# Kernel tuning notes

Hardware: AMD Instinct MI355X
Metric: run time of the kernel (lower is better)

## Reference

```python
import jax, jax.numpy as jnp
import numpy as np
import math

IN_C = 768
CA = 384
K1 = (3, 1, 1)
K2 = (1, 3, 3)
K3 = (3, 3, 3)


def _dwconv3d(x, w, b):
    # x: [B, Ca, T, H, W]; w: [Ca, 1, kt, kh, kw]; depthwise (groups = Ca)
    pads = [(k // 2, k // 2) for k in w.shape[2:]]
    y = jax.lax.conv_general_dilated(
        x, w, window_strides=(1, 1, 1), padding=pads,
        feature_group_count=x.shape[1],
        dimension_numbers=("NCDHW", "OIDHW", "NCDHW"))
    return y + b[None, :, None, None, None]


def setup_inputs() -> dict:
    key = jax.random.key(0)
    ks = jax.random.split(key, 12)
    s = 0.02
    x = jax.random.normal(ks[0], (128, 197, IN_C), dtype=jnp.float32)
    fc1_w = jax.random.normal(ks[1], (CA, IN_C), dtype=jnp.float32) * s
    fc1_b = jnp.zeros((CA,), dtype=jnp.float32)
    conv1_w = jax.random.normal(ks[2], (CA, 1) + K1, dtype=jnp.float32) * s
    conv1_b = jax.random.normal(ks[3], (CA,), dtype=jnp.float32) * s
    conv2_w = jax.random.normal(ks[4], (CA, 1) + K2, dtype=jnp.float32) * s
    conv2_b = jax.random.normal(ks[5], (CA,), dtype=jnp.float32) * s
    conv3_w = jax.random.normal(ks[6], (CA, 1) + K3, dtype=jnp.float32) * s
    conv3_b = jax.random.normal(ks[7], (CA,), dtype=jnp.float32) * s
    proj_w = jax.random.normal(ks[8], (CA, 1) + K1, dtype=jnp.float32) * s
    proj_b = jax.random.normal(ks[9], (CA,), dtype=jnp.float32) * s
    fc2_w = jax.random.normal(ks[10], (IN_C, CA), dtype=jnp.float32) * s
    fc2_b = jnp.zeros((IN_C,), dtype=jnp.float32)
    return {
        "x": x, "fc1_w": fc1_w, "fc1_b": fc1_b,
        "conv1_w": conv1_w, "conv1_b": conv1_b,
        "conv2_w": conv2_w, "conv2_b": conv2_b,
        "conv3_w": conv3_w, "conv3_b": conv3_b,
        "proj_w": proj_w, "proj_b": proj_b,
        "fc2_w": fc2_w, "fc2_b": fc2_b,
        "T": 16,
    }


def reference(x, fc1_w, fc1_b, conv1_w, conv1_b, conv2_w, conv2_b,
              conv3_w, conv3_b, proj_w, proj_b, fc2_w, fc2_b, T):
    BT, L, C = x.shape
    B = BT // T
    H = W = round(math.sqrt(L - 1))
    Ca = fc1_w.shape[0]
    x_id = x
    # drop CLS token, project down: [BT, L-1, Ca]
    h = jnp.einsum("blc,ac->bla", x[:, 1:, :], fc1_w) + fc1_b
    # [B, Ca, T, H, W]
    h = h.reshape(B, T, H, W, Ca).transpose(0, 4, 1, 2, 3)
    identity = h
    h = (_dwconv3d(h, conv1_w, conv1_b)
         + _dwconv3d(h, conv2_w, conv2_b)
         + _dwconv3d(h, conv3_w, conv3_b)) / 3.0
    h = h + identity
    h = h + _dwconv3d(h, proj_w, proj_b)
    # back to tokens: [BT, L-1, Ca]
    h = h.transpose(0, 2, 3, 4, 1).reshape(BT, L - 1, Ca)
    h = jnp.einsum("bla,ca->blc", h, fc2_w) + fc2_b
    return x_id.at[:, 1:, :].add(h)
```

## Files before the change

kernel.cpp:

```cpp
#include <hip/hip_runtime.h>
#include <cstdint>

typedef __bf16 bf16_t;
typedef __bf16 bf16x4 __attribute__((ext_vector_type(4)));
typedef __bf16 bf16x8 __attribute__((ext_vector_type(8)));
typedef float f32x4 __attribute__((ext_vector_type(4)));

#define BT_   128
#define LTOK  197
#define CIN   768
#define CA_   384
#define TT    16
#define HH    14
#define NTOK  25088

__device__ __forceinline__ void gl_lds16(const void* g, void* l) {
  __builtin_amdgcn_global_load_lds(
      (const __attribute__((address_space(1))) unsigned int*)g,
      (__attribute__((address_space(3))) unsigned int*)l,
      16, 0, 0);
}

#define SBAR() do { __builtin_amdgcn_sched_barrier(0); \
                    __builtin_amdgcn_s_barrier(); \
                    __builtin_amdgcn_sched_barrier(0); } while (0)

__global__ void prep_weights_kernel(
    const float* __restrict__ c1w, const float* __restrict__ c1b,
    const float* __restrict__ c2w, const float* __restrict__ c2b,
    const float* __restrict__ c3w, const float* __restrict__ c3b,
    const float* __restrict__ projw,
    bf16_t* __restrict__ Wtb,
    float* __restrict__ beff,
    float* __restrict__ pwt) {
  int a = blockIdx.x * blockDim.x + threadIdx.x;
  if (a >= CA_) return;
  for (int dt = 0; dt < 3; dt++)
    for (int dh = 0; dh < 3; dh++)
      for (int dw = 0; dw < 3; dw++) {
        float v = c3w[a*27 + dt*9 + dh*3 + dw];
        if (dh == 1 && dw == 1) v += c1w[a*3 + dt];
        if (dt == 1)            v += c2w[a*9 + dh*3 + dw];
        v *= (1.0f/3.0f);
        if (dt == 1 && dh == 1 && dw == 1) v += 1.0f;
        Wtb[((dt*3+dh)*3+dw)*CA_ + a] = (bf16_t)v;
      }
  beff[a] = (c1b[a] + c2b[a] + c3b[a]) * (1.0f/3.0f);
  pwt[0*CA_ + a] = projw[a*3 + 0];
  pwt[1*CA_ + a] = projw[a*3 + 1];
  pwt[2*CA_ + a] = projw[a*3 + 2];
}

__global__ __launch_bounds__(256) void convert_w_kernel(
    const float* __restrict__ fc1w, const float* __restrict__ fc2w,
    const float* __restrict__ x, float* __restrict__ out,
    bf16_t* __restrict__ W1, bf16_t* __restrict__ W2,
    bf16_t* __restrict__ xb) {
  const int NW1 = CA_*CIN/4;
  const int NW2 = CIN*CA_/4;
  const int NX  = BT_*LTOK*CIN/4;
  const int total = NW1 + NW2 + NX;
  for (int i = blockIdx.x*256 + threadIdx.x; i < total; i += gridDim.x*256) {
    if (i < NW1) {
      float4 v = ((const float4*)fc1w)[i];
      bf16x4 b; b[0]=(bf16_t)v.x; b[1]=(bf16_t)v.y; b[2]=(bf16_t)v.z; b[3]=(bf16_t)v.w;
      *(bf16x4*)(W1 + (size_t)i*4) = b;
    } else if (i < NW1 + NW2) {
      int j = i - NW1;
      float4 v = ((const float4*)fc2w)[j];
      bf16x4 b; b[0]=(bf16_t)v.x; b[1]=(bf16_t)v.y; b[2]=(bf16_t)v.z; b[3]=(bf16_t)v.w;
      *(bf16x4*)(W2 + (size_t)j*4) = b;
    } else {
      int j = i - NW1 - NW2;
      int row = j / 192;
      int c4  = j - row*192;
      int l   = row % 197;
      float4 v = ((const float4*)x)[(size_t)j];
      if (l == 0) {
        ((float4*)out)[(size_t)j] = v;
      } else {
        int tok = (row/197)*196 + (l - 1);
        bf16x4 b; b[0]=(bf16_t)v.x; b[1]=(bf16_t)v.y; b[2]=(bf16_t)v.z; b[3]=(bf16_t)v.w;
        *(bf16x4*)(xb + (size_t)tok*CIN + c4*4) = b;
      }
    }
  }
}

__global__ __launch_bounds__(256) void gemm1_kernel(
    const bf16_t* __restrict__ xb, const bf16_t* __restrict__ W1,
    const float* __restrict__ fc1b, bf16_t* __restrict__ H0) {
  __shared__ bf16_t Alds[3][128*32];
  __shared__ bf16_t Blds[3][128*32];
  const int tid  = threadIdx.x;
  const int lane = tid & 63;
  const int wave = tid >> 6;
  const int bm = blockIdx.x, bn = blockIdx.y;

  const bf16_t* asrc0 = xb + (size_t)(bm*128 + (tid>>2))*CIN + (tid&3)*8;
  const bf16_t* asrc1 = asrc0 + (size_t)64*CIN;
  const bf16_t* bsrc0 = W1 + (size_t)(bn*128 + (tid>>2))*CIN + (tid&3)*8;
  const bf16_t* bsrc1 = bsrc0 + (size_t)64*CIN;
  const int off0 = tid*8;
  const int off1 = (tid+256)*8;

  const int quad = lane >> 4;
  const int r16  = lane & 15;
  const int wm = (wave >> 1) * 64;
  const int wn = (wave & 1) * 64;

  f32x4 acc[4][4] = {};

#define G1_G(S, K) do { \
    gl_lds16(asrc0 + (K), &Alds[S][off0]); \
    gl_lds16(asrc1 + (K), &Alds[S][off1]); \
    gl_lds16(bsrc0 + (K), &Blds[S][off0]); \
    gl_lds16(bsrc1 + (K), &Blds[S][off1]); } while (0)
#define G1_M(S) do { bf16x8 af_[4], bf_[4]; \
    _Pragma("unroll") \
    for (int mt = 0; mt < 4; mt++) \
      af_[mt] = *(const bf16x8*)&Alds[S][(wm + mt*16 + r16)*32 + quad*8]; \
    _Pragma("unroll") \
    for (int nt = 0; nt < 4; nt++) \
      bf_[nt] = *(const bf16x8*)&Blds[S][(wn + nt*16 + r16)*32 + quad*8]; \
    _Pragma("unroll") \
    for (int mt = 0; mt < 4; mt++) \
      _Pragma("unroll") \
      for (int nt = 0; nt < 4; nt++) \
        acc[mt][nt] = __builtin_amdgcn_mfma_f32_16x16x32_bf16(af_[mt], bf_[nt], acc[mt][nt], 0, 0, 0); \
  } while (0)

  G1_G(0, 0);
  G1_G(1, 32);
  asm volatile("s_waitcnt vmcnt(4)" ::: "memory");
  SBAR();

  #pragma unroll 1
  for (int ii = 0; ii < 7; ii++) {
    #pragma unroll
    for (int j = 0; j < 3; j++) {
      const int i = ii*3 + j;
      G1_G((j + 2) % 3, (i + 2)*32);
      G1_M(j);
      asm volatile("s_waitcnt vmcnt(4)" ::: "memory");
      SBAR();
    }
  }
  G1_G(2, 23*32);
  G1_M(0);
  asm volatile("s_waitcnt vmcnt(4)" ::: "memory");
  SBAR();
  G1_M(1);
  asm volatile("s_waitcnt vmcnt(0)" ::: "memory");
  SBAR();
  G1_M(2);

  #pragma unroll
  for (int nt = 0; nt < 4; nt++) {
    const int col = bn*128 + wn + nt*16 + r16;
    const float bias = fc1b[col];
    #pragma unroll
    for (int mt = 0; mt < 4; mt++) {
      const int row0 = bm*128 + wm + mt*16 + quad*4;
      #pragma unroll
      for (int rg = 0; rg < 4; rg++)
        H0[(size_t)(row0 + rg)*CA_ + col] = (bf16_t)(acc[mt][nt][rg] + bias);
    }
  }
#undef G1_G
#undef G1_M
}

__global__ __launch_bounds__(192) void conv_kernel(
    const bf16_t* __restrict__ H0,
    const bf16_t* __restrict__ Wtb,
    const float* __restrict__ beff,
    const float* __restrict__ pwt,
    const float* __restrict__ pb,
    bf16_t* __restrict__ Z) {
  __shared__ bf16_t Wlds[27*CA_];
  __shared__ float  ybuf[2][2][CA_];

  const int tid = threadIdx.x;
  {
    const uint4* src = (const uint4*)Wtb;
    uint4* dst = (uint4*)Wlds;
    #pragma unroll
    for (int i = 0; i < 7; i++) {
      int idx = tid + i*192;
      if (idx < 27*CA_/8) dst[idx] = src[idx];
    }
  }

  const int blk  = blockIdx.x;
  const int b    = blk & 7;
  const int pair = blk >> 3;
  const int cg   = tid % 48;
  const int ct   = tid / 48;
  const int col  = ct >> 1;
  const int th   = ct & 1;
  const int hw   = pair*2 + col;
  const int h    = hw / HH, w = hw % HH;
  const int c0   = cg * 8;
  const int t0   = th * 8;

  float y[8][8];
  {
    f32x4 bv0 = *(const f32x4*)(beff + c0);
    f32x4 bv1 = *(const f32x4*)(beff + c0 + 4);
    #pragma unroll
    for (int i = 0; i < 8; i++) {
      #pragma unroll
      for (int c = 0; c < 4; c++) { y[i][c] = bv0[c]; y[i][c+4] = bv1[c]; }
    }
  }

  __syncthreads();

  const size_t rowstride = (size_t)196*CA_;
  const bf16_t* base_t0 = H0 + ((size_t)(b*TT + t0)*196)*CA_ + c0;
  const int tau_e_off = th ? -1 : 8;

  for (int j = 0; j < 9; j++) {
    const int dh = j / 3, dw = j - dh*3;
    const int h2 = h + dh - 1, w2 = w + dw - 1;
    const bool ok = ((unsigned)h2 < HH) && ((unsigned)w2 < HH);
    const int sp = ok ? (h2*HH + w2) : hw;
    const float m = ok ? 1.0f : 0.0f;

    const bf16x8 wv0 = *(const bf16x8*)&Wlds[(0*9+j)*CA_ + c0];
    const bf16x8 wv1 = *(const bf16x8*)&Wlds[(1*9+j)*CA_ + c0];
    const bf16x8 wv2 = *(const bf16x8*)&Wlds[(2*9+j)*CA_ + c0];
    float mw0[8], mw1[8], mw2[8];
    #pragma unroll
    for (int c = 0; c < 8; c++) {
      mw0[c] = m * (float)wv0[c];
      mw1[c] = m * (float)wv1[c];
      mw2[c] = m * (float)wv2[c];
    }

    const bf16_t* tp = base_t0 + (size_t)sp*CA_;
    bf16x8 gv[8];
    #pragma unroll
    for (int i = 0; i < 8; i++)
      gv[i] = *(const bf16x8*)(tp + (ptrdiff_t)i*(ptrdiff_t)rowstride);
    const bf16x8 ge = *(const bf16x8*)(tp + (ptrdiff_t)tau_e_off*(ptrdiff_t)rowstride);

    #pragma unroll
    for (int i = 0; i < 8; i++) {
      float gf[8];
      #pragma unroll
      for (int c = 0; c < 8; c++) gf[c] = (float)gv[i][c];
      #pragma unroll
      for (int c = 0; c < 8; c++) y[i][c] += gf[c]*mw1[c];
      if (i > 0) {
        #pragma unroll
        for (int c = 0; c < 8; c++) y[i-1][c] += gf[c]*mw2[c];
      }
      if (i < 7) {
        #pragma unroll
        for (int c = 0; c < 8; c++) y[i+1][c] += gf[c]*mw0[c];
      }
    }
    {
      float gf[8];
      #pragma unroll
      for (int c = 0; c < 8; c++) gf[c] = (float)ge[c];
      if (th) {
        #pragma unroll
        for (int c = 0; c < 8; c++) y[0][c] += gf[c]*mw0[c];
      } else {
        #pragma unroll
        for (int c = 0; c < 8; c++) y[7][c] += gf[c]*mw2[c];
      }
    }
  }

  #pragma unroll
  for (int c = 0; c < 8; c++) ybuf[col][th][c0+c] = th ? y[0][c] : y[7][c];
  __syncthreads();
  float yedge[8];
  #pragma unroll
  for (int c = 0; c < 8; c++) yedge[c] = ybuf[col][1-th][c0+c];

  float p0[8], p1[8], p2[8], pbv[8];
  {
    f32x4 a0 = *(const f32x4*)(pwt + 0*CA_ + c0), a1 = *(const f32x4*)(pwt + 0*CA_ + c0 + 4);
    f32x4 b0 = *(const f32x4*)(pwt + 1*CA_ + c0), b1 = *(const f32x4*)(pwt + 1*CA_ + c0 + 4);
    f32x4 d0 = *(const f32x4*)(pwt + 2*CA_ + c0), d1 = *(const f32x4*)(pwt + 2*CA_ + c0 + 4);
    f32x4 e0 = *(const f32x4*)(pb + c0),          e1 = *(const f32x4*)(pb + c0 + 4);
    #pragma unroll
    for (int c = 0; c < 4; c++) {
      p0[c]=a0[c]; p0[c+4]=a1[c];
      p1[c]=b0[c]; p1[c+4]=b1[c];
      p2[c]=d0[c]; p2[c+4]=d1[c];
      pbv[c]=e0[c]; pbv[c+4]=e1[c];
    }
  }

  bf16_t* zbase = Z + ((size_t)(b*TT + t0)*196 + hw)*CA_ + c0;
  #pragma unroll
  for (int i = 0; i < 8; i++) {
    bf16x8 zo;
    #pragma unroll
    for (int c = 0; c < 8; c++) {
      const float ym = (i > 0) ? y[i-1][c] : (th ? yedge[c] : 0.f);
      const float yp = (i < 7) ? y[i+1][c] : (th ? 0.f : yedge[c]);
      const float z  = y[i][c] + pbv[c] + p0[c]*ym + p1[c]*y[i][c] + p2[c]*yp;
      zo[c] = (bf16_t)z;
    }
    *(bf16x8*)(zbase + (size_t)i*rowstride) = zo;
  }
}

__global__ __launch_bounds__(256) void gemm2_kernel(
    const bf16_t* __restrict__ Z, const bf16_t* __restrict__ W2,
    const float* __restrict__ fc2b, const float* __restrict__ x,
    float* __restrict__ out) {
  __shared__ bf16_t Alds[3][128*32];
  __shared__ bf16_t Blds[3][128*32];
  const int tid  = threadIdx.x;
  const int lane = tid & 63;
  const int wave = tid >> 6;
  const int bm = blockIdx.x, bn = blockIdx.y;

  const bf16_t* asrc0 = Z  + (size_t)(bm*128 + (tid>>2))*CA_ + (tid&3)*8;
  const bf16_t* asrc1 = asrc0 + (size_t)64*CA_;
  const bf16_t* bsrc0 = W2 + (size_t)(bn*128 + (tid>>2))*CA_ + (tid&3)*8;
  const bf16_t* bsrc1 = bsrc0 + (size_t)64*CA_;
  const int off0 = tid*8;
  const int off1 = (tid+256)*8;

  const int quad = lane >> 4;
  const int r16  = lane & 15;
  const int wm = (wave >> 1) * 64;
  const int wn = (wave & 1) * 64;

  f32x4 acc[4][4] = {};

#define G2_G(S, K) do { \
    gl_lds16(asrc0 + (K), &Alds[S][off0]); \
    gl_lds16(asrc1 + (K), &Alds[S][off1]); \
    gl_lds16(bsrc0 + (K), &Blds[S][off0]); \
    gl_lds16(bsrc1 + (K), &Blds[S][off1]); } while (0)
#define G2_M(S) do { bf16x8 af_[4], bf_[4]; \
    _Pragma("unroll") \
    for (int mt = 0; mt < 4; mt++) \
      af_[mt] = *(const bf16x8*)&Alds[S][(wm + mt*16 + r16)*32 + quad*8]; \
    _Pragma("unroll") \
    for (int nt = 0; nt < 4; nt++) \
      bf_[nt] = *(const bf16x8*)&Blds[S][(wn + nt*16 + r16)*32 + quad*8]; \
    _Pragma("unroll") \
    for (int mt = 0; mt < 4; mt++) \
      _Pragma("unroll") \
      for (int nt = 0; nt < 4; nt++) \
        acc[mt][nt] = __builtin_amdgcn_mfma_f32_16x16x32_bf16(af_[mt], bf_[nt], acc[mt][nt], 0, 0, 0); \
  } while (0)

  G2_G(0, 0);
  G2_G(1, 32);
  asm volatile("s_waitcnt vmcnt(4)" ::: "memory");
  SBAR();

  #pragma unroll 1
  for (int ii = 0; ii < 3; ii++) {
    #pragma unroll
    for (int j = 0; j < 3; j++) {
      const int i = ii*3 + j;
      G2_G((j + 2) % 3, (i + 2)*32);
      G2_M(j);
      asm volatile("s_waitcnt vmcnt(4)" ::: "memory");
      SBAR();
    }
  }
  G2_G(2, 11*32);
  G2_M(0);
  asm volatile("s_waitcnt vmcnt(4)" ::: "memory");
  SBAR();
  G2_M(1);
  asm volatile("s_waitcnt vmcnt(0)" ::: "memory");
  SBAR();
  G2_M(2);

  #pragma unroll
  for (int nt = 0; nt < 4; nt++) {
    const int col = bn*128 + wn + nt*16 + r16;
    const float bias = fc2b[col];
    #pragma unroll
    for (int mt = 0; mt < 4; mt++) {
      #pragma unroll
      for (int rg = 0; rg < 4; rg++) {
        const int tok = bm*128 + wm + mt*16 + quad*4 + rg;
        const int bt  = tok / 196;
        const size_t o = (size_t)(tok + bt + 1)*CIN + col;
        out[o] = x[o] + acc[mt][nt][rg] + bias;
      }
    }
  }
#undef G2_G
#undef G2_M
}

extern "C" void kernel_launch(void* const* d_in, const int* in_sizes, int n_in,
                              void* d_out, int out_size, void* d_ws, size_t ws_size,
                              hipStream_t stream) {
  (void)in_sizes; (void)n_in; (void)out_size; (void)ws_size;
  const float* x    = (const float*)d_in[0];
  const float* fc1w = (const float*)d_in[1];
  const float* fc1b = (const float*)d_in[2];
  const float* c1w  = (const float*)d_in[3];
  const float* c1b  = (const float*)d_in[4];
  const float* c2w  = (const float*)d_in[5];
  const float* c2b  = (const float*)d_in[6];
  const float* c3w  = (const float*)d_in[7];
  const float* c3b  = (const float*)d_in[8];
  const float* pw   = (const float*)d_in[9];
  const float* pb   = (const float*)d_in[10];
  const float* fc2w = (const float*)d_in[11];
  const float* fc2b = (const float*)d_in[12];
  float* out = (float*)d_out;

  char* ws = (char*)d_ws;
  bf16_t* W1   = (bf16_t*)(ws);
  bf16_t* W2   = (bf16_t*)(ws + 589824);
  bf16_t* Wtb  = (bf16_t*)(ws + 1179648);
  float*  beff = (float*) (ws + 1200384);
  float*  pwt  = (float*) (ws + 1201920);
  bf16_t* xb   = (bf16_t*)(ws + 1206528);
  bf16_t* Z    = (bf16_t*)(ws + 1206528);
  bf16_t* H0   = (bf16_t*)(ws + 39741696);

  prep_weights_kernel<<<dim3(2), dim3(192), 0, stream>>>(
      c1w, c1b, c2w, c2b, c3w, c3b, pw, Wtb, beff, pwt);
  convert_w_kernel<<<dim3(4096), dim3(256), 0, stream>>>(fc1w, fc2w, x, out, W1, W2, xb);
  gemm1_kernel<<<dim3(196, 3), dim3(256), 0, stream>>>(xb, W1, fc1b, H0);
  conv_kernel<<<dim3(784), dim3(192), 0, stream>>>(H0, Wtb, beff, pwt, pb, Z);
  gemm2_kernel<<<dim3(196, 6), dim3(256), 0, stream>>>(Z, W2, fc2b, x, out);
}
```

Baseline: 279.5 us.

## Pre-swizzle GEMM weights into MFMA fragment layout and load B directly to registers

The weight conversion now writes fc1/fc2 into a fragment-ordered layout, so each lane can fetch its MFMA B operand with one contiguous 16-byte global load. Both GEMMs drop the B tile from LDS and load B fragments straight into registers each k-step. This halves LDS traffic and the global-to-LDS copies per stage and frees LDS for occupancy. In exchange, B loads now come from global or L2 memory with less time to hide their latency, and each of the two waves in a column pair fetches the same weights.

```diff
diff --git a/kernel.cpp b/kernel.cpp
--- a/kernel.cpp
+++ b/kernel.cpp
@@ -54,7 +54,7 @@
 __global__ __launch_bounds__(256) void convert_w_kernel(
     const float* __restrict__ fc1w, const float* __restrict__ fc2w,
     const float* __restrict__ x, float* __restrict__ out,
-    bf16_t* __restrict__ W1, bf16_t* __restrict__ W2,
+    bf16_t* __restrict__ W1f, bf16_t* __restrict__ W2f,
     bf16_t* __restrict__ xb) {
   const int NW1 = CA_*CIN/4;
   const int NW2 = CIN*CA_/4;
@@ -62,14 +62,21 @@
   const int total = NW1 + NW2 + NX;
   for (int i = blockIdx.x*256 + threadIdx.x; i < total; i += gridDim.x*256) {
     if (i < NW1) {
-      float4 v = ((const float4*)fc1w)[i];
+      int e = i*4, f = e >> 9, t = e & 511, l = t >> 3, jb = t & 7;
+      int ch = f / 24, cb = f - ch*24;
+      int col = cb*16 + (l & 15);
+      int k   = ch*32 + ((l >> 4) << 3) + jb;
+      float4 v = *(const float4*)(fc1w + (size_t)col*CIN + k);
       bf16x4 b; b[0]=(bf16_t)v.x; b[1]=(bf16_t)v.y; b[2]=(bf16_t)v.z; b[3]=(bf16_t)v.w;
-      *(bf16x4*)(W1 + (size_t)i*4) = b;
+      *(bf16x4*)(W1f + e) = b;
     } else if (i < NW1 + NW2) {
-      int j = i - NW1;
-      float4 v = ((const float4*)fc2w)[j];
+      int e = (i - NW1)*4, f = e >> 9, t = e & 511, l = t >> 3, jb = t & 7;
+      int ch = f / 48, cb = f - ch*48;
+      int col = cb*16 + (l & 15);
+      int k   = ch*32 + ((l >> 4) << 3) + jb;
+      float4 v = *(const float4*)(fc2w + (size_t)col*CA_ + k);
       bf16x4 b; b[0]=(bf16_t)v.x; b[1]=(bf16_t)v.y; b[2]=(bf16_t)v.z; b[3]=(bf16_t)v.w;
-      *(bf16x4*)(W2 + (size_t)j*4) = b;
+      *(bf16x4*)(W2f + e) = b;
     } else {
       int j = i - NW1 - NW2;
       int row = j / 192;
@@ -88,10 +95,9 @@
 }
 
 __global__ __launch_bounds__(256) void gemm1_kernel(
-    const bf16_t* __restrict__ xb, const bf16_t* __restrict__ W1,
+    const bf16_t* __restrict__ xb, const bf16_t* __restrict__ W1f,
     const float* __restrict__ fc1b, bf16_t* __restrict__ H0) {
-  __shared__ bf16_t Alds[3][128*32];
-  __shared__ bf16_t Blds[3][128*32];
+  __shared__ bf16_t Alds[3][4096];
   const int tid  = threadIdx.x;
   const int lane = tid & 63;
   const int wave = tid >> 6;
@@ -99,40 +105,40 @@
 
   const bf16_t* asrc0 = xb + (size_t)(bm*128 + (tid>>2))*CIN + (tid&3)*8;
   const bf16_t* asrc1 = asrc0 + (size_t)64*CIN;
-  const bf16_t* bsrc0 = W1 + (size_t)(bn*128 + (tid>>2))*CIN + (tid&3)*8;
-  const bf16_t* bsrc1 = bsrc0 + (size_t)64*CIN;
   const int off0 = tid*8;
-  const int off1 = (tid+256)*8;
+  const int off1 = tid*8 + 2048;
 
   const int quad = lane >> 4;
   const int r16  = lane & 15;
   const int wm = (wave >> 1) * 64;
   const int wn = (wave & 1) * 64;
 
+  const bf16_t* wb = W1f + ((size_t)(bn*8 + (wave & 1)*4))*512 + lane*8;
+
   f32x4 acc[4][4] = {};
 
-#define G1_G(S, K) do { \
+#define G1_A(S, K) do { \
     gl_lds16(asrc0 + (K), &Alds[S][off0]); \
-    gl_lds16(asrc1 + (K), &Alds[S][off1]); \
-    gl_lds16(bsrc0 + (K), &Blds[S][off0]); \
-    gl_lds16(bsrc1 + (K), &Blds[S][off1]); } while (0)
-#define G1_M(S) do { bf16x8 af_[4], bf_[4]; \
+    gl_lds16(asrc1 + (K), &Alds[S][off1]); } while (0)
+#define G1_B(CH) do { \
+    bfr[0] = *(const bf16x8*)(wb + (size_t)((CH)*24 + 0)*512); \
+    bfr[1] = *(const bf16x8*)(wb + (size_t)((CH)*24 + 1)*512); \
+    bfr[2] = *(const bf16x8*)(wb + (size_t)((CH)*24 + 2)*512); \
+    bfr[3] = *(const bf16x8*)(wb + (size_t)((CH)*24 + 3)*512); } while (0)
+#define G1_M(S) do { bf16x8 af_[4]; \
     _Pragma("unroll") \
     for (int mt = 0; mt < 4; mt++) \
       af_[mt] = *(const bf16x8*)&Alds[S][(wm + mt*16 + r16)*32 + quad*8]; \
     _Pragma("unroll") \
-    for (int nt = 0; nt < 4; nt++) \
-      bf_[nt] = *(const bf16x8*)&Blds[S][(wn + nt*16 + r16)*32 + quad*8]; \
-    _Pragma("unroll") \
     for (int mt = 0; mt < 4; mt++) \
       _Pragma("unroll") \
       for (int nt = 0; nt < 4; nt++) \
-        acc[mt][nt] = __builtin_amdgcn_mfma_f32_16x16x32_bf16(af_[mt], bf_[nt], acc[mt][nt], 0, 0, 0); \
+        acc[mt][nt] = __builtin_amdgcn_mfma_f32_16x16x32_bf16(af_[mt], bfr[nt], acc[mt][nt], 0, 0, 0); \
   } while (0)
 
-  G1_G(0, 0);
-  G1_G(1, 32);
-  asm volatile("s_waitcnt vmcnt(4)" ::: "memory");
+  G1_A(0, 0);
+  G1_A(1, 32);
+  asm volatile("s_waitcnt vmcnt(2)" ::: "memory");
   SBAR();
 
   #pragma unroll 1
@@ -140,20 +146,37 @@
     #pragma unroll
     for (int j = 0; j < 3; j++) {
       const int i = ii*3 + j;
-      G1_G((j + 2) % 3, (i + 2)*32);
+      bf16x8 bfr[4];
+      G1_B(i);
+      __builtin_amdgcn_sched_barrier(0);
+      G1_A((j + 2) % 3, (i + 2)*32);
       G1_M(j);
-      asm volatile("s_waitcnt vmcnt(4)" ::: "memory");
+      asm volatile("s_waitcnt vmcnt(2)" ::: "memory");
       SBAR();
     }
   }
-  G1_G(2, 23*32);
-  G1_M(0);
-  asm volatile("s_waitcnt vmcnt(4)" ::: "memory");
-  SBAR();
-  G1_M(1);
-  asm volatile("s_waitcnt vmcnt(0)" ::: "memory");
-  SBAR();
-  G1_M(2);
+  {
+    bf16x8 bfr[4];
+    G1_B(21);
+    __builtin_amdgcn_sched_barrier(0);
+    G1_A(2, 23*32);
+    G1_M(0);
+    asm volatile("s_waitcnt vmcnt(2)" ::: "memory");
+    SBAR();
+  }
+  {
+    bf16x8 bfr[4];
+    G1_B(22);
+    __builtin_amdgcn_sched_barrier(0);
+    G1_M(1);
+    asm volatile("s_waitcnt vmcnt(0)" ::: "memory");
+    SBAR();
+  }
+  {
+    bf16x8 bfr[4];
+    G1_B(23);
+    G1_M(2);
+  }
 
   #pragma unroll
   for (int nt = 0; nt < 4; nt++) {
@@ -167,7 +190,8 @@
         H0[(size_t)(row0 + rg)*CA_ + col] = (bf16_t)(acc[mt][nt][rg] + bias);
     }
   }
-#undef G1_G
+#undef G1_A
+#undef G1_B
 #undef G1_M
 }
 
@@ -314,52 +338,51 @@
 }
 
 __global__ __launch_bounds__(256) void gemm2_kernel(
-    const bf16_t* __restrict__ Z, const bf16_t* __restrict__ W2,
+    const bf16_t* __restrict__ Z, const bf16_t* __restrict__ W2f,
     const float* __restrict__ fc2b, const float* __restrict__ x,
     float* __restrict__ out) {
-  __shared__ bf16_t Alds[3][128*32];
-  __shared__ bf16_t Blds[3][128*32];
+  __shared__ bf16_t Alds[3][4096];
   const int tid  = threadIdx.x;
   const int lane = tid & 63;
   const int wave = tid >> 6;
   const int bm = blockIdx.x, bn = blockIdx.y;
 
-  const bf16_t* asrc0 = Z  + (size_t)(bm*128 + (tid>>2))*CA_ + (tid&3)*8;
+  const bf16_t* asrc0 = Z + (size_t)(bm*128 + (tid>>2))*CA_ + (tid&3)*8;
   const bf16_t* asrc1 = asrc0 + (size_t)64*CA_;
-  const bf16_t* bsrc0 = W2 + (size_t)(bn*128 + (tid>>2))*CA_ + (tid&3)*8;
-  const bf16_t* bsrc1 = bsrc0 + (size_t)64*CA_;
   const int off0 = tid*8;
-  const int off1 = (tid+256)*8;
+  const int off1 = tid*8 + 2048;
 
   const int quad = lane >> 4;
   const int r16  = lane & 15;
   const int wm = (wave >> 1) * 64;
   const int wn = (wave & 1) * 64;
 
+  const bf16_t* wb = W2f + ((size_t)(bn*8 + (wave & 1)*4))*512 + lane*8;
+
   f32x4 acc[4][4] = {};
 
-#define G2_G(S, K) do { \
+#define G2_A(S, K) do { \
     gl_lds16(asrc0 + (K), &Alds[S][off0]); \
-    gl_lds16(asrc1 + (K), &Alds[S][off1]); \
-    gl_lds16(bsrc0 + (K), &Blds[S][off0]); \
-    gl_lds16(bsrc1 + (K), &Blds[S][off1]); } while (0)
-#define G2_M(S) do { bf16x8 af_[4], bf_[4]; \
+    gl_lds16(asrc1 + (K), &Alds[S][off1]); } while (0)
+#define G2_B(CH) do { \
+    bfr[0] = *(const bf16x8*)(wb + (size_t)((CH)*48 + 0)*512); \
+    bfr[1] = *(const bf16x8*)(wb + (size_t)((CH)*48 + 1)*512); \
+    bfr[2] = *(const bf16x8*)(wb + (size_t)((CH)*48 + 2)*512); \
+    bfr[3] = *(const bf16x8*)(wb + (size_t)((CH)*48 + 3)*512); } while (0)
+#define G2_M(S) do { bf16x8 af_[4]; \
     _Pragma("unroll") \
     for (int mt = 0; mt < 4; mt++) \
       af_[mt] = *(const bf16x8*)&Alds[S][(wm + mt*16 + r16)*32 + quad*8]; \
     _Pragma("unroll") \
-    for (int nt = 0; nt < 4; nt++) \
-      bf_[nt] = *(const bf16x8*)&Blds[S][(wn + nt*16 + r16)*32 + quad*8]; \
-    _Pragma("unroll") \
     for (int mt = 0; mt < 4; mt++) \
       _Pragma("unroll") \
       for (int nt = 0; nt < 4; nt++) \
-        acc[mt][nt] = __builtin_amdgcn_mfma_f32_16x16x32_bf16(af_[mt], bf_[nt], acc[mt][nt], 0, 0, 0); \
+        acc[mt][nt] = __builtin_amdgcn_mfma_f32_16x16x32_bf16(af_[mt], bfr[nt], acc[mt][nt], 0, 0, 0); \
   } while (0)
 
-  G2_G(0, 0);
-  G2_G(1, 32);
-  asm volatile("s_waitcnt vmcnt(4)" ::: "memory");
+  G2_A(0, 0);
+  G2_A(1, 32);
+  asm volatile("s_waitcnt vmcnt(2)" ::: "memory");
   SBAR();
 
   #pragma unroll 1
@@ -367,20 +390,37 @@
     #pragma unroll
     for (int j = 0; j < 3; j++) {
       const int i = ii*3 + j;
-      G2_G((j + 2) % 3, (i + 2)*32);
+      bf16x8 bfr[4];
+      G2_B(i);
+      __builtin_amdgcn_sched_barrier(0);
+      G2_A((j + 2) % 3, (i + 2)*32);
       G2_M(j);
-      asm volatile("s_waitcnt vmcnt(4)" ::: "memory");
+      asm volatile("s_waitcnt vmcnt(2)" ::: "memory");
       SBAR();
     }
   }
-  G2_G(2, 11*32);
-  G2_M(0);
-  asm volatile("s_waitcnt vmcnt(4)" ::: "memory");
-  SBAR();
-  G2_M(1);
-  asm volatile("s_waitcnt vmcnt(0)" ::: "memory");
-  SBAR();
-  G2_M(2);
+  {
+    bf16x8 bfr[4];
+    G2_B(9);
+    __builtin_amdgcn_sched_barrier(0);
+    G2_A(2, 11*32);
+    G2_M(0);
+    asm volatile("s_waitcnt vmcnt(2)" ::: "memory");
+    SBAR();
+  }
+  {
+    bf16x8 bfr[4];
+    G2_B(10);
+    __builtin_amdgcn_sched_barrier(0);
+    G2_M(1);
+    asm volatile("s_waitcnt vmcnt(0)" ::: "memory");
+    SBAR();
+  }
+  {
+    bf16x8 bfr[4];
+    G2_B(11);
+    G2_M(2);
+  }
 
   #pragma unroll
   for (int nt = 0; nt < 4; nt++) {
@@ -397,7 +437,8 @@
       }
     }
   }
-#undef G2_G
+#undef G2_A
+#undef G2_B
 #undef G2_M
 }
 
@@ -421,8 +462,8 @@
   float* out = (float*)d_out;
 
   char* ws = (char*)d_ws;
-  bf16_t* W1   = (bf16_t*)(ws);
-  bf16_t* W2   = (bf16_t*)(ws + 589824);
+  bf16_t* W1f  = (bf16_t*)(ws);
+  bf16_t* W2f  = (bf16_t*)(ws + 589824);
   bf16_t* Wtb  = (bf16_t*)(ws + 1179648);
   float*  beff = (float*) (ws + 1200384);
   float*  pwt  = (float*) (ws + 1201920);
@@ -432,8 +473,8 @@
 
   prep_weights_kernel<<<dim3(2), dim3(192), 0, stream>>>(
       c1w, c1b, c2w, c2b, c3w, c3b, pw, Wtb, beff, pwt);
-  convert_w_kernel<<<dim3(4096), dim3(256), 0, stream>>>(fc1w, fc2w, x, out, W1, W2, xb);
-  gemm1_kernel<<<dim3(196, 3), dim3(256), 0, stream>>>(xb, W1, fc1b, H0);
+  convert_w_kernel<<<dim3(4096), dim3(256), 0, stream>>>(fc1w, fc2w, x, out, W1f, W2f, xb);
+  gemm1_kernel<<<dim3(196, 3), dim3(256), 0, stream>>>(xb, W1f, fc1b, H0);
   conv_kernel<<<dim3(784), dim3(192), 0, stream>>>(H0, Wtb, beff, pwt, pb, Z);
-  gemm2_kernel<<<dim3(196, 6), dim3(256), 0, stream>>>(Z, W2, fc2b, x, out);
-}
+  gemm2_kernel<<<dim3(196, 6), dim3(256), 0, stream>>>(Z, W2f, fc2b, x, out);
+}
```

After: 266.3 us. 1.05x faster.
